# Optimization experiments

Measured on AMD Instinct MI355X. Metric: run time of the kernel, lower is better.

The kernel has to match this reference:

```python
import jax, jax.numpy as jnp
import numpy as np
from jax import lax

DIVISOR = 2.0


def setup_inputs() -> dict:
    key = jax.random.key(0)
    k1, k2, k3, k4 = jax.random.split(key, 4)
    x = jax.random.normal(k1, (128, 8, 32, 32, 32), dtype=jnp.float32)
    conv_weight = jax.random.normal(k2, (16, 8, 3, 3, 3), dtype=jnp.float32) * 0.1
    conv_bias = jax.random.normal(k3, (16,), dtype=jnp.float32) * 0.1
    bias = jax.random.normal(k4, (16, 1, 1, 1), dtype=jnp.float32) * 0.1
    return {"x": x, "conv_weight": conv_weight, "conv_bias": conv_bias, "bias": bias}


def reference(x, conv_weight, conv_bias, bias):
    # Conv3d, stride 1, no padding: [B,8,32,32,32] -> [B,16,30,30,30]
    y = lax.conv_general_dilated(
        x, conv_weight,
        window_strides=(1, 1, 1), padding='VALID',
        dimension_numbers=('NCDHW', 'OIDHW', 'NCDHW'))
    y = y + conv_bias[None, :, None, None, None]
    # divide by scalar divisor
    y = y / DIVISOR
    # MaxPool3d kernel=stride=2: [B,16,30,30,30] -> [B,16,15,15,15]
    y = lax.reduce_window(
        y, -jnp.inf, lax.max,
        window_dimensions=(1, 1, 2, 2, 2),
        window_strides=(1, 1, 2, 2, 2),
        padding='VALID')
    # AdaptiveAvgPool3d((1,1,1)): global mean over D,H,W -> [B,16,1,1,1]
    y = jnp.mean(y, axis=(2, 3, 4), keepdims=True)
    # bias add (bias shape [16,1,1,1] broadcasts over batch)
    y = y + bias
    # sum over channel dim (dim=1) -> [B,1,1,1]
    return jnp.sum(y, axis=1)
```

## Files before the change

kernel.cpp:

```cpp
#include <hip/hip_runtime.h>


using short8 = __attribute__((ext_vector_type(8))) short;
using f32x16 = __attribute__((ext_vector_type(16))) float;

__device__ __forceinline__ unsigned short f2bf(float f) {
  unsigned u = __float_as_uint(f);
  return (unsigned short)((u + 0x7FFFu + ((u >> 16) & 1u)) >> 16);
}

__global__ __launch_bounds__(256) void prep_w(const float* __restrict__ cw,
                                              short* __restrict__ Bp) {
  int i = threadIdx.x + blockIdx.x * 256;
  if (i >= 1152) return;
  int g = i >> 6, l = i & 63;
  int pb2 = g / 9, kh = (g / 3) % 3, kw = g % 3;
  int col = l & 31, koff = l >> 5;
  int co = col & 15, od = col >> 4;
  int kd = 2 * pb2 + koff - od;
  short8 o;
#pragma unroll
  for (int j = 0; j < 8; ++j) {
    float v = (kd >= 0 && kd <= 2) ? cw[(co * 8 + j) * 27 + kd * 9 + kh * 3 + kw] : 0.0f;
    o[j] = (short)f2bf(v);
  }
  *(short8*)(Bp + (size_t)i * 8) = o;
}

__global__ __launch_bounds__(512, 2) void conv_mfma(const float* __restrict__ x,
                                                    const short* __restrict__ Bp,
                                                    float* __restrict__ partial) {
  __shared__ __align__(16) char lds[6 * 16384];
  __shared__ float red[8];
  const int blk = blockIdx.x;
  const int b = blk >> 1, dh = blk & 1;
  const int t = threadIdx.x, lane = t & 63, wv = t >> 6;
  const int pd0 = dh ? 7 : 0;
  const int nst = dh ? 8 : 7;
  const int plane0 = 2 * pd0;
  const float* xb = x + (size_t)b * 262144;

  const int ow = lane & 31, koff = lane >> 5, hi = lane >> 5;
  int wbv[3];
#pragma unroll
  for (int kw = 0; kw < 3; ++kw) {
    int w = ow + kw; if (w > 31) w = 31;
    wbv[kw] = (w * 16) ^ (((w >> 3) & 3) << 4);
  }

  const int sh = t >> 4, swq = (t >> 1) & 7, sch = t & 1;
  const float* gbase = xb + (size_t)(sch * 4) * 32768 + sh * 32 + swq * 4;

  auto loadSite = [&](int d, float4& v0, float4& v1, float4& v2, float4& v3) {
    const float* gp = gbase + d * 1024;
    v0 = *(const float4*)(gp);
    v1 = *(const float4*)(gp + 32768);
    v2 = *(const float4*)(gp + 65536);
    v3 = *(const float4*)(gp + 98304);
  };
  auto storeSite = [&](int d, const float4& v0, const float4& v1, const float4& v2,
                       const float4& v3) {
    char* sb = lds + (d % 6) * 16384 + sh * 512 + sch * 8;
    const float* a0 = (const float*)&v0; const float* a1 = (const float*)&v1;
    const float* a2 = (const float*)&v2; const float* a3 = (const float*)&v3;
#pragma unroll
    for (int j = 0; j < 4; ++j) {
      int w = swq * 4 + j;
      int wbyte = (w * 16) ^ (((w >> 3) & 3) << 4);
      uint2 val;
      val.x = (unsigned)f2bf(a0[j]) | ((unsigned)f2bf(a1[j]) << 16);
      val.y = (unsigned)f2bf(a2[j]) | ((unsigned)f2bf(a3[j]) << 16);
      *(uint2*)(sb + wbyte) = val;
    }
  };

#pragma unroll
  for (int pr = 0; pr < 4; ++pr) {
    float4 v0, v1, v2, v3;
    loadSite(plane0 + pr, v0, v1, v2, v3);
    storeSite(plane0 + pr, v0, v1, v2, v3);
  }

  short8 Bw[18];
#pragma unroll
  for (int g = 0; g < 18; ++g)
    Bw[g] = *(const short8*)(Bp + ((size_t)g * 64 + lane) * 8);

  __syncthreads();

  float sum = 0.0f;
  for (int st = 0; st < nst; ++st) {
    const int pd = pd0 + st;
    const bool more = (st < nst - 1);
    const int dpair = 2 * pd + 4;

    int b6 = (2 * pd) % 6;
    int s0 = b6 + koff; if (s0 >= 6) s0 -= 6;
    int s1 = b6 + 2 + koff; if (s1 >= 6) s1 -= 6;
    char* lp0 = lds + s0 * 16384;
    char* lp1 = lds + s1 * 16384;

    auto chunk = [&](int q) {
      const int oh0 = 2 * q;
      short8 fS[4][6];
#pragma unroll
      for (int j = 0; j < 4; ++j) {
        char* r0 = lp0 + (oh0 + j) * 512;
        char* r1 = lp1 + (oh0 + j) * 512;
#pragma unroll
        for (int kw = 0; kw < 3; ++kw) {
          fS[j][kw]     = *(const short8*)(r0 + wbv[kw]);
          fS[j][3 + kw] = *(const short8*)(r1 + wbv[kw]);
        }
      }
      f32x16 C[2] = {};
#pragma unroll
      for (int pb2 = 0; pb2 < 2; ++pb2)
#pragma unroll
        for (int kh = 0; kh < 3; ++kh)
#pragma unroll
          for (int kw = 0; kw < 3; ++kw) {
            const int fi = pb2 * 3 + kw;
            const int g = (pb2 * 3 + kh) * 3 + kw;
            C[0] = __builtin_amdgcn_mfma_f32_32x32x16_bf16(fS[kh][fi], Bw[g], C[0], 0, 0, 0);
            C[1] = __builtin_amdgcn_mfma_f32_32x32x16_bf16(fS[kh + 1][fi], Bw[g], C[1], 0, 0, 0);
          }
      float part = 0.0f;
#pragma unroll
      for (int i = 0; i < 8; ++i) {
        float v = fmaxf(fmaxf(C[0][2 * i], C[0][2 * i + 1]),
                        fmaxf(C[1][2 * i], C[1][2 * i + 1]));
        v = fmaxf(v, __shfl_xor(v, 16));
        if (((lane & 31) < 16) && !(hi == 1 && i == 7)) part += v;
      }
      sum += part;
    };

    float4 v0, v1, v2, v3;
    if (more) loadSite(dpair, v0, v1, v2, v3);

    chunk(wv);

    if (more) {
      storeSite(dpair, v0, v1, v2, v3);
      loadSite(dpair + 1, v0, v1, v2, v3);
    }

    if (wv < 7) chunk(wv + 8);

    if (more) storeSite(dpair + 1, v0, v1, v2, v3);

    __syncthreads();
  }

#pragma unroll
  for (int off = 32; off; off >>= 1) sum += __shfl_down(sum, off);
  if (lane == 0) red[wv] = sum;
  __syncthreads();
  if (t == 0) {
    float s2 = 0.0f;
#pragma unroll
    for (int i = 0; i < 8; ++i) s2 += red[i];
    partial[blk] = s2;
  }
}

__global__ __launch_bounds__(128) void finalize(const float* __restrict__ partial,
                                                const float* __restrict__ cb,
                                                const float* __restrict__ bias,
                                                float* __restrict__ out) {
  int b = threadIdx.x;
  if (b >= 128) return;
  float k = 0.0f;
#pragma unroll
  for (int c = 0; c < 16; ++c) k += cb[c] * 0.5f + bias[c];
  out[b] = (partial[2 * b] + partial[2 * b + 1]) * (1.0f / 6750.0f) + k;
}

extern "C" void kernel_launch(void* const* d_in, const int* in_sizes, int n_in,
                              void* d_out, int out_size, void* d_ws, size_t ws_size,
                              hipStream_t stream) {
  const float* x    = (const float*)d_in[0];
  const float* cw   = (const float*)d_in[1];
  const float* cb   = (const float*)d_in[2];
  const float* bias = (const float*)d_in[3];
  float* out = (float*)d_out;

  short* Bp      = (short*)d_ws;
  float* partial = (float*)((char*)d_ws + 32768);

  prep_w<<<5, 256, 0, stream>>>(cw, Bp);
  conv_mfma<<<256, 512, 0, stream>>>(x, Bp, partial);
  finalize<<<1, 128, 0, stream>>>(partial, cb, bias, out);
}
```

Baseline: 50.14 us.

## Split conv work by H-row quarters across 512 smaller blocks with slimmer LDS slabs

```diff
diff --git a/kernel.cpp b/kernel.cpp
--- a/kernel.cpp
+++ b/kernel.cpp
@@ -4,7 +4,7 @@
 using short8 = __attribute__((ext_vector_type(8))) short;
 using f32x16 = __attribute__((ext_vector_type(16))) float;
 
-__device__ __forceinline__ unsigned short f2bf(float f) {
+__device__ __forceinline__ unsigned short f2bf_rn(float f) {
   unsigned u = __float_as_uint(f);
   return (unsigned short)((u + 0x7FFFu + ((u >> 16) & 1u)) >> 16);
 }
@@ -22,159 +22,144 @@
 #pragma unroll
   for (int j = 0; j < 8; ++j) {
     float v = (kd >= 0 && kd <= 2) ? cw[(co * 8 + j) * 27 + kd * 9 + kh * 3 + kw] : 0.0f;
-    o[j] = (short)f2bf(v);
+    o[j] = (short)f2bf_rn(v);
   }
   *(short8*)(Bp + (size_t)i * 8) = o;
 }
 
-__global__ __launch_bounds__(512, 2) void conv_mfma(const float* __restrict__ x,
+__global__ __launch_bounds__(256, 2) void conv_mfma(const float* __restrict__ x,
                                                     const short* __restrict__ Bp,
                                                     float* __restrict__ partial) {
-  __shared__ __align__(16) char lds[6 * 16384];
-  __shared__ float red[8];
-  const int blk = blockIdx.x;
-  const int b = blk >> 1, dh = blk & 1;
+  __shared__ __align__(16) char lds[6 * 5120];
+  __shared__ float red[4];
+
+  const int bid = blockIdx.x;
+  const int swz = (bid & 7) * 64 + (bid >> 3);
+  const int b = swz >> 2, q = swz & 3;
   const int t = threadIdx.x, lane = t & 63, wv = t >> 6;
-  const int pd0 = dh ? 7 : 0;
-  const int nst = dh ? 8 : 7;
-  const int plane0 = 2 * pd0;
+  const int nph = (q == 3) ? 3 : 4;
+  const int nrows = (q == 3) ? 8 : 10;
+  const int row0 = 8 * q;
+  const int sites = nrows * 8;
   const float* xb = x + (size_t)b * 262144;
 
-  const int ow = lane & 31, koff = lane >> 5, hi = lane >> 5;
+  const bool sact = t < 2 * sites;
+  const int spl = (t >= sites) ? 1 : 0;
+  const int ss = sact ? (t - spl * sites) : 0;
+  const int shr = ss >> 3, swc = ss & 7;
+  const float* gsite = xb + (row0 + shr) * 32 + swc * 4;
+
+  auto issue = [&](int dpair, float4* v) {
+    if (!sact) return;
+    const float* gp = gsite + (dpair + spl) * 1024;
+#pragma unroll
+    for (int ci = 0; ci < 8; ++ci) v[ci] = *(const float4*)(gp + ci * 32768);
+  };
+  auto writeSlab = [&](int dpair, const float4* v) {
+    if (!sact) return;
+    const int d = dpair + spl;
+    char* sb = lds + (d % 6) * 5120 + shr * 512;
+#pragma unroll
+    for (int wi = 0; wi < 4; ++wi) {
+      const int w = swc * 4 + wi;
+      uint4 o;
+      o.x = __builtin_amdgcn_perm(__float_as_uint(((const float*)&v[1])[wi]),
+                                  __float_as_uint(((const float*)&v[0])[wi]), 0x07060302u);
+      o.y = __builtin_amdgcn_perm(__float_as_uint(((const float*)&v[3])[wi]),
+                                  __float_as_uint(((const float*)&v[2])[wi]), 0x07060302u);
+      o.z = __builtin_amdgcn_perm(__float_as_uint(((const float*)&v[5])[wi]),
+                                  __float_as_uint(((const float*)&v[4])[wi]), 0x07060302u);
+      o.w = __builtin_amdgcn_perm(__float_as_uint(((const float*)&v[7])[wi]),
+                                  __float_as_uint(((const float*)&v[6])[wi]), 0x07060302u);
+      *(uint4*)(sb + ((w * 16) ^ (((w >> 3) & 3) << 4))) = o;
+    }
+  };
+
+  const int ow = lane & 31, koff = lane >> 5;
   int wbv[3];
 #pragma unroll
   for (int kw = 0; kw < 3; ++kw) {
     int w = ow + kw; if (w > 31) w = 31;
     wbv[kw] = (w * 16) ^ (((w >> 3) & 3) << 4);
   }
-
-  const int sh = t >> 4, swq = (t >> 1) & 7, sch = t & 1;
-  const float* gbase = xb + (size_t)(sch * 4) * 32768 + sh * 32 + swq * 4;
-
-  auto loadSite = [&](int d, float4& v0, float4& v1, float4& v2, float4& v3) {
-    const float* gp = gbase + d * 1024;
-    v0 = *(const float4*)(gp);
-    v1 = *(const float4*)(gp + 32768);
-    v2 = *(const float4*)(gp + 65536);
-    v3 = *(const float4*)(gp + 98304);
-  };
-  auto storeSite = [&](int d, const float4& v0, const float4& v1, const float4& v2,
-                       const float4& v3) {
-    char* sb = lds + (d % 6) * 16384 + sh * 512 + sch * 8;
-    const float* a0 = (const float*)&v0; const float* a1 = (const float*)&v1;
-    const float* a2 = (const float*)&v2; const float* a3 = (const float*)&v3;
-#pragma unroll
-    for (int j = 0; j < 4; ++j) {
-      int w = swq * 4 + j;
-      int wbyte = (w * 16) ^ (((w >> 3) & 3) << 4);
-      uint2 val;
-      val.x = (unsigned)f2bf(a0[j]) | ((unsigned)f2bf(a1[j]) << 16);
-      val.y = (unsigned)f2bf(a2[j]) | ((unsigned)f2bf(a3[j]) << 16);
-      *(uint2*)(sb + wbyte) = val;
-    }
-  };
-
-#pragma unroll
-  for (int pr = 0; pr < 4; ++pr) {
-    float4 v0, v1, v2, v3;
-    loadSite(plane0 + pr, v0, v1, v2, v3);
-    storeSite(plane0 + pr, v0, v1, v2, v3);
-  }
+  const bool docomp = wv < nph;
+  const int rowb = 2 * wv;
 
   short8 Bw[18];
 #pragma unroll
   for (int g = 0; g < 18; ++g)
     Bw[g] = *(const short8*)(Bp + ((size_t)g * 64 + lane) * 8);
 
+  {
+    float4 va[8], vb[8];
+    issue(0, va); issue(2, vb);
+    writeSlab(0, va); writeSlab(2, vb);
+  }
   __syncthreads();
 
   float sum = 0.0f;
-  for (int st = 0; st < nst; ++st) {
-    const int pd = pd0 + st;
-    const bool more = (st < nst - 1);
-    const int dpair = 2 * pd + 4;
+  int slot0 = koff, slot1 = 2 + koff;
+  for (int pd = 0; pd < 15; ++pd) {
+    const bool more = (pd < 14);
+    float4 va[8];
+    if (more) issue(2 * pd + 4, va);
 
-    int b6 = (2 * pd) % 6;
-    int s0 = b6 + koff; if (s0 >= 6) s0 -= 6;
-    int s1 = b6 + 2 + koff; if (s1 >= 6) s1 -= 6;
-    char* lp0 = lds + s0 * 16384;
-    char* lp1 = lds + s1 * 16384;
-
-    auto chunk = [&](int q) {
-      const int oh0 = 2 * q;
-      short8 fS[4][6];
+    if (docomp) {
+      f32x16 C0 = {}, C1 = {};
+      const char* p0 = lds + slot0 * 5120 + rowb * 512;
+      const char* p1 = lds + slot1 * 5120 + rowb * 512;
 #pragma unroll
       for (int j = 0; j < 4; ++j) {
-        char* r0 = lp0 + (oh0 + j) * 512;
-        char* r1 = lp1 + (oh0 + j) * 512;
+        short8 f[6];
 #pragma unroll
         for (int kw = 0; kw < 3; ++kw) {
-          fS[j][kw]     = *(const short8*)(r0 + wbv[kw]);
-          fS[j][3 + kw] = *(const short8*)(r1 + wbv[kw]);
+          f[kw]     = *(const short8*)(p0 + j * 512 + wbv[kw]);
+          f[3 + kw] = *(const short8*)(p1 + j * 512 + wbv[kw]);
         }
-      }
-      f32x16 C[2] = {};
 #pragma unroll
-      for (int pb2 = 0; pb2 < 2; ++pb2)
-#pragma unroll
-        for (int kh = 0; kh < 3; ++kh)
+        for (int pb2 = 0; pb2 < 2; ++pb2)
 #pragma unroll
           for (int kw = 0; kw < 3; ++kw) {
-            const int fi = pb2 * 3 + kw;
-            const int g = (pb2 * 3 + kh) * 3 + kw;
-            C[0] = __builtin_amdgcn_mfma_f32_32x32x16_bf16(fS[kh][fi], Bw[g], C[0], 0, 0, 0);
-            C[1] = __builtin_amdgcn_mfma_f32_32x32x16_bf16(fS[kh + 1][fi], Bw[g], C[1], 0, 0, 0);
+            if (j < 3)
+              C0 = __builtin_amdgcn_mfma_f32_32x32x16_bf16(f[pb2 * 3 + kw],
+                     Bw[pb2 * 9 + j * 3 + kw], C0, 0, 0, 0);
+            if (j > 0)
+              C1 = __builtin_amdgcn_mfma_f32_32x32x16_bf16(f[pb2 * 3 + kw],
+                     Bw[pb2 * 9 + (j - 1) * 3 + kw], C1, 0, 0, 0);
           }
-      float part = 0.0f;
+      }
 #pragma unroll
       for (int i = 0; i < 8; ++i) {
-        float v = fmaxf(fmaxf(C[0][2 * i], C[0][2 * i + 1]),
-                        fmaxf(C[1][2 * i], C[1][2 * i + 1]));
+        float v = fmaxf(fmaxf(C0[2 * i], C0[2 * i + 1]),
+                        fmaxf(C1[2 * i], C1[2 * i + 1]));
         v = fmaxf(v, __shfl_xor(v, 16));
-        if (((lane & 31) < 16) && !(hi == 1 && i == 7)) part += v;
+        if (((lane & 31) < 16) && !(koff == 1 && i == 7)) sum += v;
       }
-      sum += part;
-    };
-
-    float4 v0, v1, v2, v3;
-    if (more) loadSite(dpair, v0, v1, v2, v3);
-
-    chunk(wv);
-
-    if (more) {
-      storeSite(dpair, v0, v1, v2, v3);
-      loadSite(dpair + 1, v0, v1, v2, v3);
     }
 
-    if (wv < 7) chunk(wv + 8);
-
-    if (more) storeSite(dpair + 1, v0, v1, v2, v3);
-
+    if (more) writeSlab(2 * pd + 4, va);
     __syncthreads();
+    slot0 += 2; if (slot0 >= 6) slot0 -= 6;
+    slot1 += 2; if (slot1 >= 6) slot1 -= 6;
   }
 
 #pragma unroll
   for (int off = 32; off; off >>= 1) sum += __shfl_down(sum, off);
   if (lane == 0) red[wv] = sum;
   __syncthreads();
-  if (t == 0) {
-    float s2 = 0.0f;
-#pragma unroll
-    for (int i = 0; i < 8; ++i) s2 += red[i];
-    partial[blk] = s2;
-  }
+  if (t == 0) partial[b * 4 + q] = red[0] + red[1] + red[2] + red[3];
 }
 
 __global__ __launch_bounds__(128) void finalize(const float* __restrict__ partial,
                                                 const float* __restrict__ cb,
                                                 const float* __restrict__ bias,
                                                 float* __restrict__ out) {
-  int b = threadIdx.x;
-  if (b >= 128) return;
+  const int b = threadIdx.x;
   float k = 0.0f;
 #pragma unroll
   for (int c = 0; c < 16; ++c) k += cb[c] * 0.5f + bias[c];
-  out[b] = (partial[2 * b] + partial[2 * b + 1]) * (1.0f / 6750.0f) + k;
+  out[b] = (partial[4 * b] + partial[4 * b + 1] + partial[4 * b + 2] +
+            partial[4 * b + 3]) * (1.0f / 6750.0f) + k;
 }
 
 extern "C" void kernel_launch(void* const* d_in, const int* in_sizes, int n_in,
@@ -190,6 +175,6 @@
   float* partial = (float*)((char*)d_ws + 32768);
 
   prep_w<<<5, 256, 0, stream>>>(cw, Bp);
-  conv_mfma<<<256, 512, 0, stream>>>(x, Bp, partial);
+  conv_mfma<<<512, 256, 0, stream>>>(x, Bp, partial);
   finalize<<<1, 128, 0, stream>>>(partial, cb, bias, out);
 }
```

Result: faster. 46.80 us (-6.6%).
